# Kernel optimization log

Measured on AMD Instinct MI355X. Metric: run time of the kernel, lower is better.

Reference implementation:

```python
import jax, jax.numpy as jnp
import numpy as np
from jax import lax

HID = 512
NEG = -1e30

def conv2d(x, w, pad):
    # x: [N,C,H,W], w: [O,I,kh,kw]
    return lax.conv_general_dilated(x, w, (1, 1), [(pad, pad), (pad, pad)],
                                    dimension_numbers=('NCHW', 'OIHW', 'NCHW'))

def maxpool3s2p1(x):
    return lax.reduce_window(x, -jnp.inf, lax.max, (1, 1, 3, 3), (1, 1, 2, 2),
                             [(0, 0), (0, 0), (1, 1), (1, 1)])

def setup_inputs() -> dict:
    key = jax.random.key(0)
    ks = jax.random.split(key, 12)
    N, B = 128, 16
    gid = jnp.repeat(jnp.arange(B), N // B).astype(jnp.float32)  # sorted group ids
    rois = jnp.concatenate([gid[:, None], jax.random.uniform(ks[0], (N, 4))], axis=1)
    interact_feat = jax.random.normal(ks[1], (N, 2304, 1, 16, 16), jnp.float32)
    bbox_feat = jax.random.normal(ks[2], (N, 1024, 4, 7, 7), jnp.float32)
    s = lambda k, sh: jax.random.normal(k, sh, jnp.float32) * 0.02
    return {
        'rois': rois,
        'interact_feat': interact_feat,
        'bbox_feat': bbox_feat,
        'w_reduce': s(ks[3], (HID, 2304, 1, 1)),
        'w_rsize': s(ks[4], (HID, HID, 3, 3)),
        'wq': s(ks[5], (HID, HID, 3, 3)),
        'wk': s(ks[6], (HID, HID, 3, 3)),
        'wv': s(ks[7], (HID, HID, 3, 3)),
        'w1': s(ks[8], (HID, HID, 3, 3)),
        'gamma': jnp.ones((HID,), jnp.float32),
        'beta': jnp.zeros((HID,), jnp.float32),
        'w_fc': s(ks[9], (HID, 2 * HID)),
    }

def reference(rois, interact_feat, bbox_feat, w_reduce, w_rsize, wq, wk, wv, w1, gamma, beta, w_fc):
    f = interact_feat[:, :, 0]                      # squeeze(2): [N,2304,16,16]
    f = jax.nn.relu(conv2d(f, w_reduce, 0))         # [N,512,16,16]
    f = conv2d(f, w_rsize, 0)                       # no padding -> [N,512,14,14]
    f = maxpool3s2p1(f)                             # [N,512,7,7]

    gid = rois[:, 0].astype(jnp.int32)
    mask = gid[:, None] == gid[None, :]             # [N,N] same-group mask (vectorizes ragged loop)

    q = conv2d(f, wq, 1)
    k = conv2d(f, wk, 1)
    v = conv2d(f, wv, 1)
    # per-pixel attention across rois within each group
    att = jnp.einsum('ichw,jchw->ijhw', q, k) / jnp.sqrt(jnp.asarray(HID, f.dtype))
    att = jnp.where(mask[:, :, None, None], att, NEG)
    att = jax.nn.softmax(att, axis=1)               # softmax over key rois (dim=1)
    virt = jnp.einsum('ijhw,jchw->ichw', att, v)    # [N,512,7,7]

    # GroupNorm(1, C): normalize over (C,H,W), per-channel affine
    mu = virt.mean(axis=(1, 2, 3), keepdims=True)
    var = virt.var(axis=(1, 2, 3), keepdims=True)
    virt = (virt - mu) / jnp.sqrt(var + 1e-5)
    virt = virt * gamma[None, :, None, None] + beta[None, :, None, None]
    virt = jax.nn.relu(virt)
    virt = conv2d(virt, w1, 1)                      # dropout = identity in eval

    ho = (f + virt).mean(axis=(2, 3))               # gap1 -> [N,512]
    ob = bbox_feat.mean(axis=(2, 3, 4))             # gap2 -> [N,1024]
    ob = jax.nn.relu(ob @ w_fc.T)                   # fc1 -> [N,512]
    return jnp.concatenate([ho, ob], axis=1)        # [N,1024]
```

## Files before the change

### kernel.cpp

```cpp
#include <hip/hip_runtime.h>
#include <hip/hip_bf16.h>
#include <math.h>

typedef __bf16 bf16;
typedef __bf16 v8bf __attribute__((ext_vector_type(8)));
typedef float f32x4 __attribute__((ext_vector_type(4)));

#define GLDS16(g, l) __builtin_amdgcn_global_load_lds( \
    (const __attribute__((address_space(1))) void*)(g), \
    (__attribute__((address_space(3))) void*)(l), 16, 0, 0)

__device__ __forceinline__ int xcd_swz(int bid, int nwg) {
  int xcd = bid & 7, off = bid >> 3;
  int q = nwg >> 3, r = nwg & 7;
  return (xcd < r ? xcd * (q + 1) : r * (q + 1) + (xcd - r) * q) + off;
}

#define RING_COMPUTE() do { \
  v8bf b_[4], a_[4]; \
  _Pragma("unroll") for (int _j = 0; _j < 4; ++_j) { \
    int _lr = _j * 16 + l15; \
    int _c = (wn * 64 + colb) ^ ((_lr & 7) << 4); \
    b_[_j] = *(const v8bf*)(s0 + 16384 + _lr * 128 + _c); } \
  _Pragma("unroll") for (int _i = 0; _i < 4; ++_i) { \
    int _lr = _i * 16 + l15; \
    int _c = (wm * 64 + colb) ^ ((_lr & 7) << 4); \
    a_[_i] = *(const v8bf*)(s0 + _lr * 128 + _c); } \
  __builtin_amdgcn_s_setprio(1); \
  _Pragma("unroll") for (int _i = 0; _i < 4; ++_i) \
  _Pragma("unroll") for (int _j = 0; _j < 4; ++_j) \
    acc[_i][_j] = __builtin_amdgcn_mfma_f32_16x16x32_bf16(a_[_i], b_[_j], acc[_i][_j], 0, 0, 0); \
  __builtin_amdgcn_s_setprio(0); \
  _Pragma("unroll") for (int _i = 0; _i < 4; ++_i) { \
    int _lr = (_i + 4) * 16 + l15; \
    int _c = (wm * 64 + colb) ^ ((_lr & 7) << 4); \
    a_[_i] = *(const v8bf*)(s0 + _lr * 128 + _c); } \
  __builtin_amdgcn_s_setprio(1); \
  _Pragma("unroll") for (int _i = 0; _i < 4; ++_i) \
  _Pragma("unroll") for (int _j = 0; _j < 4; ++_j) \
    acc[_i + 4][_j] = __builtin_amdgcn_mfma_f32_16x16x32_bf16(a_[_i], b_[_j], acc[_i + 4][_j], 0, 0, 0); \
  __builtin_amdgcn_s_setprio(0); \
} while (0)

#define RING_LOOP(NG, STAGE) do { \
  STAGE(0, s0); STAGE(1, s1); \
  for (int g = 0; g < (NG); ++g) { \
    if (g + 2 < (NG)) { STAGE(g + 2, s2); } \
    if (g + 2 < (NG))       asm volatile("s_waitcnt vmcnt(12)" ::: "memory"); \
    else if (g + 2 == (NG)) asm volatile("s_waitcnt vmcnt(6)" ::: "memory"); \
    else                    asm volatile("s_waitcnt vmcnt(0)" ::: "memory"); \
    __builtin_amdgcn_s_barrier(); \
    __builtin_amdgcn_sched_barrier(0); \
    RING_COMPUTE(); \
    __builtin_amdgcn_sched_barrier(0); \
    __builtin_amdgcn_s_barrier(); \
    char* _tmp = s0; s0 = s1; s1 = s2; s2 = _tmp; \
  } \
} while (0)

__global__ __launch_bounds__(256, 2)
void k_gemm_reduce(const bf16* __restrict__ A, const bf16* __restrict__ B,
                   bf16* __restrict__ f1, int mbase)
{
  __shared__ __attribute__((aligned(16))) char lds[73728];
  char *s0 = lds, *s1 = lds + 24576, *s2 = lds + 49152;
  const int s = xcd_swz(blockIdx.x, gridDim.x);
  const int by = s & 3, bx = s >> 2;
  const int t = threadIdx.x, lane = t & 63, w = t >> 6;
  const int wm = w >> 1, wn = w & 1;
  const int l15 = lane & 15, colb = (lane >> 4) << 4;
  const int tr = t >> 3;
  const int lb = ((t & 7) << 4) ^ ((tr & 7) << 4);
  const int hi = lb >> 6, kb = lb & 63;
  const int t16 = t * 16;
  const char* pa[4]; const char* pb[2];
  #pragma unroll
  for (int i = 0; i < 4; ++i)
    pa[i] = (const char*)A + (size_t)(bx * 256 + i * 32 + tr + hi * 128) * 4608 + kb;
  #pragma unroll
  for (int i = 0; i < 2; ++i)
    pb[i] = (const char*)B + (size_t)(by * 128 + i * 32 + tr + hi * 64) * 4608 + kb;
  #define SG(kt, ring) do { \
    _Pragma("unroll") for (int _i = 0; _i < 4; ++_i) \
      GLDS16(pa[_i] + (size_t)(kt) * 64, (ring) + _i * 4096 + t16); \
    _Pragma("unroll") for (int _i = 0; _i < 2; ++_i) \
      GLDS16(pb[_i] + (size_t)(kt) * 64, (ring) + 16384 + _i * 4096 + t16); } while (0)
  f32x4 acc[8][4] = {};
  RING_LOOP(72, SG);
  const int rbase = (lane >> 4) << 2, cl = lane & 15;
  #pragma unroll
  for (int i = 0; i < 8; ++i)
    #pragma unroll
    for (int j = 0; j < 4; ++j)
      #pragma unroll
      for (int r = 0; r < 4; ++r) {
        int row = mbase + bx * 256 + wm * 128 + i * 16 + rbase + r;
        int col = by * 128 + wn * 64 + j * 16 + cl;
        f1[(size_t)row * 512 + col] = (bf16)fmaxf(acc[i][j][r], 0.f);
      }
}

__global__ __launch_bounds__(256, 2)
void k_conv_rsize(const bf16* __restrict__ f1, const bf16* __restrict__ wt,
                  bf16* __restrict__ f14)
{
  __shared__ __attribute__((aligned(16))) char lds[73728];
  char *s0 = lds, *s1 = lds + 24576, *s2 = lds + 49152;
  const int s = xcd_swz(blockIdx.x, gridDim.x);
  const int by = s & 3, bx = s >> 2;
  const int t = threadIdx.x, lane = t & 63, w = t >> 6;
  const int wm = w >> 1, wn = w & 1;
  const int l15 = lane & 15, colb = (lane >> 4) << 4;
  const int tr = t >> 3;
  const int lb = ((t & 7) << 4) ^ ((tr & 7) << 4);
  const int hi = lb >> 6, kb = lb & 63;
  const int t16 = t * 16;
  int abase[4]; const char* pb[2];
  #pragma unroll
  for (int i = 0; i < 4; ++i) {
    int m = bx * 256 + i * 32 + tr + hi * 128;
    int n = m / 196, rem = m - n * 196;
    int y = rem / 14, x = rem - 14 * (rem / 14);
    abase[i] = n * 256 + y * 16 + x;
  }
  #pragma unroll
  for (int i = 0; i < 2; ++i)
    pb[i] = (const char*)wt + (size_t)(by * 128 + i * 32 + tr + hi * 64) * 1024 + kb;
  const char* f1c = (const char*)f1 + kb;
  #define SC(kt, ring) do { int _tap = (kt) >> 4, _ko = ((kt) & 15) << 6; \
    int _dy = (_tap * 11) >> 5, _dx = _tap - _dy * 3; \
    int _df = (_dy * 16 + _dx) << 10; \
    _Pragma("unroll") for (int _i = 0; _i < 4; ++_i) \
      GLDS16(f1c + ((size_t)abase[_i] << 10) + _df + _ko, (ring) + _i * 4096 + t16); \
    _Pragma("unroll") for (int _i = 0; _i < 2; ++_i) \
      GLDS16(pb[_i] + (size_t)_tap * 524288 + _ko, (ring) + 16384 + _i * 4096 + t16); } while (0)
  f32x4 acc[8][4] = {};
  RING_LOOP(144, SC);
  const int rbase = (lane >> 4) << 2, cl = lane & 15;
  #pragma unroll
  for (int i = 0; i < 8; ++i)
    #pragma unroll
    for (int j = 0; j < 4; ++j)
      #pragma unroll
      for (int r = 0; r < 4; ++r) {
        int row = bx * 256 + wm * 128 + i * 16 + rbase + r;
        int col = by * 128 + wn * 64 + j * 16 + cl;
        f14[(size_t)row * 512 + col] = (bf16)acc[i][j][r];
      }
}

__global__ __launch_bounds__(256, 2)
void k_conv_qkv(const bf16* __restrict__ fin, const bf16* __restrict__ wt,
                bf16* __restrict__ qkv, const bf16* __restrict__ zp,
                const float* __restrict__ bbox, float* __restrict__ obm)
{
  __shared__ __attribute__((aligned(16))) char lds[73728];
  char *s0 = lds, *s1 = lds + 24576, *s2 = lds + 49152;
  const int t = threadIdx.x;
  if (blockIdx.x >= 300) {
    int bid = blockIdx.x - 300;
    int n = bid >> 4;
    int c = (bid & 15) * 64 + (t >> 2);
    int seg = t & 3;
    const float4* p4 = (const float4*)(bbox + ((size_t)n * 1024 + c) * 196);
    float sum = 0.f;
    for (int k = seg; k < 49; k += 4) { float4 ww = p4[k]; sum += ww.x + ww.y + ww.z + ww.w; }
    sum += __shfl_xor(sum, 1);
    sum += __shfl_xor(sum, 2);
    if (seg == 0) obm[n * 1024 + c] = sum * (1.f / 196.f);
    return;
  }
  const int s = xcd_swz(blockIdx.x, 300);
  const int q12 = s % 12, bx = s / 12;
  const int tensor = q12 >> 2, byl = q12 & 3;
  const char* wtc = (const char*)wt + (size_t)tensor * 4718592;
  bf16* outp = qkv + (size_t)tensor * 3211264;
  const int lane = t & 63, w = t >> 6;
  const int wm = w >> 1, wn = w & 1;
  const int l15 = lane & 15, colb = (lane >> 4) << 4;
  const int tr = t >> 3;
  const int lb = ((t & 7) << 4) ^ ((tr & 7) << 4);
  const int hi = lb >> 6, kb = lb & 63;
  const int t16 = t * 16;
  int nb[4], py[4], px[4]; const char* pb[2];
  #pragma unroll
  for (int i = 0; i < 4; ++i) {
    int m = bx * 256 + i * 32 + tr + hi * 128;
    if (m > 6271) m = 6271;
    int n = m / 49, rem = m - n * 49;
    nb[i] = n * 49;
    py[i] = rem / 7 - 1;
    px[i] = rem - 7 * (rem / 7) - 1;
  }
  #pragma unroll
  for (int i = 0; i < 2; ++i)
    pb[i] = wtc + (size_t)(byl * 128 + i * 32 + tr + hi * 64) * 1024 + kb;
  const char* finc = (const char*)fin + kb;
  const char* zpc = (const char*)zp;
  #define SQ(kt, ring) do { int _tap = (kt) >> 4, _ko = ((kt) & 15) << 6; \
    int _dy = (_tap * 11) >> 5, _dx = _tap - _dy * 3; \
    _Pragma("unroll") for (int _i = 0; _i < 4; ++_i) { \
      int _iy = py[_i] + _dy, _ix = px[_i] + _dx; \
      const char* _sp = ((unsigned)_iy < 7u && (unsigned)_ix < 7u) \
          ? finc + (size_t)(nb[_i] + _iy * 7 + _ix) * 1024 + _ko : zpc; \
      GLDS16(_sp, (ring) + _i * 4096 + t16); } \
    _Pragma("unroll") for (int _i = 0; _i < 2; ++_i) \
      GLDS16(pb[_i] + (size_t)_tap * 524288 + _ko, (ring) + 16384 + _i * 4096 + t16); } while (0)
  f32x4 acc[8][4] = {};
  RING_LOOP(144, SQ);
  const int rbase = (lane >> 4) << 2, cl = lane & 15;
  #pragma unroll
  for (int i = 0; i < 8; ++i)
    #pragma unroll
    for (int j = 0; j < 4; ++j)
      #pragma unroll
      for (int r = 0; r < 4; ++r) {
        int row = bx * 256 + wm * 128 + i * 16 + rbase + r;
        if (row < 6272) {
          int col = byl * 128 + wn * 64 + j * 16 + cl;
          outp[(size_t)row * 512 + col] = (bf16)acc[i][j][r];
        }
      }
}

__device__ __forceinline__ void tile_compute(const char* ldsA, const char* ldsB,
                                             f32x4 (&acc)[4][4], int wr, int wc, int lane) {
  const int l15 = lane & 15;
  const int colb = (lane >> 4) << 4;
  #pragma unroll
  for (int kk = 0; kk < 2; ++kk) {
    v8bf a[4], b[4];
    #pragma unroll
    for (int i = 0; i < 4; ++i) {
      int ra = wr * 64 + i * 16 + l15;
      int ca = ((kk << 6) | colb) ^ ((ra & 7) << 4);
      a[i] = *(const v8bf*)(ldsA + ra * 128 + ca);
    }
    #pragma unroll
    for (int j = 0; j < 4; ++j) {
      int rb = wc * 64 + j * 16 + l15;
      int cb = ((kk << 6) | colb) ^ ((rb & 7) << 4);
      b[j] = *(const v8bf*)(ldsB + rb * 128 + cb);
    }
    __builtin_amdgcn_s_setprio(1);
    #pragma unroll
    for (int i = 0; i < 4; ++i)
      #pragma unroll
      for (int j = 0; j < 4; ++j)
        acc[i][j] = __builtin_amdgcn_mfma_f32_16x16x32_bf16(a[i], b[j], acc[i][j], 0, 0, 0);
    __builtin_amdgcn_s_setprio(0);
  }
}

#define PIPELINE_LOOP(NK)                                                   \
  stage(0, lds);                                                            \
  stage(1, lds + 32768);                                                    \
  int cur = 0;                                                              \
  for (int ks = 0; ks < (NK) - 1; ++ks) {                                   \
    asm volatile("s_waitcnt vmcnt(8)" ::: "memory");                        \
    __builtin_amdgcn_s_barrier();                                           \
    __builtin_amdgcn_sched_barrier(0);                                      \
    tile_compute(lds + cur * 32768, lds + cur * 32768 + 16384, acc, wr, wc, lane); \
    __builtin_amdgcn_sched_barrier(0);                                      \
    __builtin_amdgcn_s_barrier();                                           \
    __builtin_amdgcn_sched_barrier(0);                                      \
    if (ks + 2 < (NK)) stage(ks + 2, lds + cur * 32768);                    \
    cur ^= 1;                                                               \
  }                                                                         \
  asm volatile("s_waitcnt vmcnt(0)" ::: "memory");                          \
  __builtin_amdgcn_s_barrier();                                             \
  __builtin_amdgcn_sched_barrier(0);                                        \
  tile_compute(lds + cur * 32768, lds + cur * 32768 + 16384, acc, wr, wc, lane);

__global__ __launch_bounds__(256)
void k_gemm_s(const bf16* __restrict__ A_s, const bf16* __restrict__ w1r,
              float* __restrict__ part)
{
  __shared__ __attribute__((aligned(16))) char lds[65536];
  const int by = blockIdx.x, kspl = blockIdx.y;
  const int t = threadIdx.x, lane = t & 63, w = t >> 6, wr = w >> 1, wc = w & 1;
  const int tr = t >> 3;
  const int cphys = ((t & 7) << 4) ^ ((tr & 7) << 4);
  const char* pa[4]; const char* pb[4];
  #pragma unroll
  for (int i = 0; i < 4; ++i) {
    int r = i * 32 + tr;
    pa[i] = (const char*)A_s + (size_t)r * 9216 + kspl * 2304 + cphys;
    pb[i] = (const char*)w1r + (size_t)(by * 128 + r) * 9216 + kspl * 2304 + cphys;
  }
  const int lo = t * 16;
  auto stage = [&](int ks, char* base) {
    #pragma unroll
    for (int i = 0; i < 4; ++i) GLDS16(pa[i] + ks * 128, base + lo + i * 4096);
    #pragma unroll
    for (int i = 0; i < 4; ++i) GLDS16(pb[i] + ks * 128, base + 16384 + lo + i * 4096);
  };
  f32x4 acc[4][4] = {};
  PIPELINE_LOOP(18)
  const int rb = (lane >> 4) << 2, cl = lane & 15;
  #pragma unroll
  for (int i = 0; i < 4; ++i)
    #pragma unroll
    for (int j = 0; j < 4; ++j)
      #pragma unroll
      for (int r = 0; r < 4; ++r) {
        int row = wr * 64 + i * 16 + rb + r;
        int col = by * 128 + wc * 64 + j * 16 + cl;
        part[(size_t)kspl * 65536 + row * 512 + col] = acc[i][j][r];
      }
}

__global__ __launch_bounds__(512)
void k_red(const float* __restrict__ part, const float* __restrict__ f7m,
           float* __restrict__ out)
{
  int idx = blockIdx.x * 512 + threadIdx.x;
  float s = part[idx] + part[65536 + idx] + part[131072 + idx] + part[196608 + idx];
  int row = idx >> 9, col = idx & 511;
  out[row * 1024 + col] = s + f7m[idx];
}

__global__ void k_tin(const float* __restrict__ in, bf16* __restrict__ A1, int n0)
{
  __shared__ float tile[64][36];
  const int k0 = blockIdx.x * 64, p0 = blockIdx.y * 32, nl = blockIdx.z;
  const int n = n0 + nl;
  const int t = threadIdx.x;
  const float* src = in + (size_t)n * 2304 * 256;
  #pragma unroll
  for (int rep = 0; rep < 2; ++rep) {
    int idx = t + rep * 256;
    int row = idx >> 3, c4 = (idx & 7) * 4;
    float4 v = *(const float4*)(src + (size_t)(k0 + row) * 256 + p0 + c4);
    tile[row][c4] = v.x; tile[row][c4 + 1] = v.y;
    tile[row][c4 + 2] = v.z; tile[row][c4 + 3] = v.w;
  }
  __syncthreads();
  const int pl = t >> 3, ke = (t & 7) * 8;
  v8bf o;
  #pragma unroll
  for (int e = 0; e < 8; ++e) o[e] = (bf16)tile[ke + e][pl];
  bf16* dst = A1 + (size_t)nl * 256 * 2304;
  *(v8bf*)(dst + (size_t)(p0 + pl) * 2304 + k0 + ke) = o;
}

__global__ void k_wprep(const float* __restrict__ wred, const float* __restrict__ s0,
                        const float* __restrict__ s1, const float* __restrict__ s2,
                        const float* __restrict__ s3, const float* __restrict__ s4,
                        bf16* __restrict__ wrb, bf16* __restrict__ wt,
                        bf16* __restrict__ w1r)
{
  if (blockIdx.x < 1152) {
    int idx = (blockIdx.x * 256 + threadIdx.x) * 4;
    float4 v = *(const float4*)(wred + idx);
    bf16* d = wrb + idx;
    d[0] = (bf16)v.x; d[1] = (bf16)v.y; d[2] = (bf16)v.z; d[3] = (bf16)v.w;
    return;
  }
  int bid = blockIdx.x - 1152;
  int by = bid >> 10, bx = bid & 1023;
  const float* src;
  switch (by) {
    case 0: src = s0; break; case 1: src = s1; break; case 2: src = s2; break;
    case 3: src = s3; break; default: src = s4; break;
  }
  int q = bx * 256 + threadIdx.x;
  const float* sp = src + (size_t)q * 9;
  float tmp[9];
  #pragma unroll
  for (int e = 0; e < 9; ++e) tmp[e] = sp[e];
  if (by < 4) {
    bf16* dst = wt + (size_t)by * 2359296;
    #pragma unroll
    for (int e = 0; e < 9; ++e) dst[(size_t)e * 262144 + q] = (bf16)tmp[e];
  } else {
    int co = q >> 9, ci = q & 511;
    #pragma unroll
    for (int e = 0; e < 9; ++e) w1r[(size_t)(co * 9 + e) * 512 + ci] = (bf16)tmp[e];
  }
}

__global__ void k_pool(const bf16* __restrict__ f14, bf16* __restrict__ f7b)
{
  int idx = blockIdx.x * 256 + threadIdx.x;
  int c2 = idx & 255;
  int pp = idx >> 8;
  int n = pp / 49, p7 = pp - n * 49;
  int y = p7 / 7, x = p7 - 7 * (p7 / 7);
  int y0 = 2 * y - 1, x0 = 2 * x - 1;
  const unsigned* f14u = (const unsigned*)f14;
  float m0 = -3.4e38f, m1 = -3.4e38f;
  #pragma unroll
  for (int dy = 0; dy < 3; ++dy) {
    int iy = y0 + dy; if ((unsigned)iy >= 14u) continue;
    #pragma unroll
    for (int dx = 0; dx < 3; ++dx) {
      int ix = x0 + dx; if ((unsigned)ix >= 14u) continue;
      unsigned vv = f14u[(size_t)(n * 196 + iy * 14 + ix) * 256 + c2];
      m0 = fmaxf(m0, __builtin_bit_cast(float, vv << 16));
      m1 = fmaxf(m1, __builtin_bit_cast(float, vv & 0xffff0000u));
    }
  }
  bf16 b0 = (bf16)m0, b1 = (bf16)m1;
  unsigned pk = (unsigned)__builtin_bit_cast(unsigned short, b0)
              | ((unsigned)__builtin_bit_cast(unsigned short, b1) << 16);
  ((unsigned*)f7b)[idx] = pk;
}

__global__ __launch_bounds__(256)
void k_attn(const bf16* __restrict__ q, const bf16* __restrict__ k,
            const bf16* __restrict__ v, const float* __restrict__ rois,
            float* __restrict__ virt)
{
  const int p = blockIdx.x, g = blockIdx.y, t = threadIdx.x;
  __shared__ float sS[8][9];
  __shared__ float sP[8][9];
  __shared__ __attribute__((aligned(16))) bf16 sV[8][512];
  {
    int u = t;
    #pragma unroll
    for (int rep = 0; rep < 2; ++rep, u += 256) {
      int j = u >> 6, ch = u & 63;
      *(v8bf*)&sV[j][ch * 8] = *(const v8bf*)(v + ((size_t)(g * 8 + j) * 49 + p) * 512 + ch * 8);
    }
  }
  int pi = t >> 2, ls = t & 3;
  int i = pi >> 3, j = pi & 7;
  const bf16* qi = q + ((size_t)(g * 8 + i) * 49 + p) * 512;
  const bf16* kj = k + ((size_t)(g * 8 + j) * 49 + p) * 512;
  float s = 0.f;
  for (int ch = ls * 16; ch < ls * 16 + 16; ++ch) {
    v8bf a = *(const v8bf*)(qi + ch * 8);
    v8bf b = *(const v8bf*)(kj + ch * 8);
    #pragma unroll
    for (int e = 0; e < 8; ++e) s += (float)a[e] * (float)b[e];
  }
  s += __shfl_xor(s, 1);
  s += __shfl_xor(s, 2);
  if (ls == 0) sS[i][j] = s * 0.04419417382415922f;
  __syncthreads();
  if (t < 8) {
    float gi = rois[(g * 8 + t) * 5];
    float pv[8]; float mx = -3.4e38f;
    #pragma unroll
    for (int jj = 0; jj < 8; ++jj) {
      float gj = rois[(g * 8 + jj) * 5];
      float sv = (gi == gj) ? sS[t][jj] : -1e30f;
      pv[jj] = sv; mx = fmaxf(mx, sv);
    }
    float sum = 0.f;
    #pragma unroll
    for (int jj = 0; jj < 8; ++jj) { float e = expf(pv[jj] - mx); pv[jj] = e; sum += e; }
    float inv = 1.f / sum;
    #pragma unroll
    for (int jj = 0; jj < 8; ++jj) sP[t][jj] = pv[jj] * inv;
  }
  __syncthreads();
  int i2 = t >> 5, c0 = (t & 31) * 16;
  float o[16];
  #pragma unroll
  for (int e = 0; e < 16; ++e) o[e] = 0.f;
  #pragma unroll
  for (int jj = 0; jj < 8; ++jj) {
    float ww = sP[i2][jj];
    v8bf v0 = *(const v8bf*)&sV[jj][c0];
    v8bf v1 = *(const v8bf*)&sV[jj][c0 + 8];
    #pragma unroll
    for (int e = 0; e < 8; ++e) { o[e] += ww * (float)v0[e]; o[8 + e] += ww * (float)v1[e]; }
  }
  float* dst = virt + ((size_t)(g * 8 + i2) * 49 + p) * 512 + c0;
  #pragma unroll
  for (int e = 0; e < 16; ++e) dst[e] = o[e];
}

__global__ __launch_bounds__(512)
void k_ln_fc(const float* __restrict__ virt, const float* __restrict__ gamma,
             const float* __restrict__ beta, const bf16* __restrict__ f7b,
             bf16* __restrict__ A_s, float* __restrict__ f7m,
             const float* __restrict__ obm, const float* __restrict__ wfc,
             float* __restrict__ out)
{
  const int t = threadIdx.x;
  if (blockIdx.x >= 128) {
    __shared__ float sO[1024];
    int n = blockIdx.x - 128;
    for (int u = t; u < 1024; u += 512) sO[u] = obm[n * 1024 + u];
    __syncthreads();
    const float4* wp = (const float4*)(wfc + (size_t)t * 1024);
    float s = 0.f;
    for (int c4 = 0; c4 < 256; ++c4) {
      float4 w = wp[c4];
      s += w.x * sO[c4 * 4] + w.y * sO[c4 * 4 + 1] + w.z * sO[c4 * 4 + 2] + w.w * sO[c4 * 4 + 3];
    }
    out[n * 1024 + 512 + t] = fmaxf(s, 0.f);
    return;
  }
  const int n = blockIdx.x;
  const float* p = virt + (size_t)n * 25088 + t;
  float xv[49];
  float s1 = 0.f, s2 = 0.f;
  #pragma unroll
  for (int pp = 0; pp < 49; ++pp) {
    float x = p[pp * 512];
    xv[pp] = x; s1 += x; s2 += x * x;
  }
  __shared__ float r1[512], r2[512];
  r1[t] = s1; r2[t] = s2; __syncthreads();
  for (int off = 256; off; off >>= 1) {
    if (t < off) { r1[t] += r1[t + off]; r2[t] += r2[t + off]; }
    __syncthreads();
  }
  float mu = r1[0] * (1.f / 25088.f);
  float var = r2[0] * (1.f / 25088.f) - mu * mu;
  float rstd = rsqrtf(var + 1e-5f);
  float g = gamma[t], be = beta[t];
  const bf16* fp = f7b + (size_t)n * 25088 + t;
  float T = 0, R0 = 0, R6 = 0, C0 = 0, C6 = 0;
  float X00 = 0, X06 = 0, X60 = 0, X66 = 0, F = 0;
  #pragma unroll
  for (int pp = 0; pp < 49; ++pp) {
    const int u = pp / 7, v = pp - 7 * (pp / 7);
    float y = fmaxf((xv[pp] - mu) * rstd * g + be, 0.f);
    T += y;
    if (u == 0) R0 += y;
    if (u == 6) R6 += y;
    if (v == 0) C0 += y;
    if (v == 6) C6 += y;
    if (pp == 0)  X00 = y;
    if (pp == 6)  X06 = y;
    if (pp == 42) X60 = y;
    if (pp == 48) X66 = y;
    F += (float)fp[pp * 512];
  }
  float sv[9] = { T-R6-C6+X66, T-R6, T-R6-C0+X60,
                  T-C6,        T,    T-C0,
                  T-R0-C6+X06, T-R0, T-R0-C0+X00 };
  bf16* Ap = A_s + (size_t)n * 4608 + t;
  #pragma unroll
  for (int tap = 0; tap < 9; ++tap)
    Ap[tap * 512] = (bf16)(sv[tap] * (1.f / 49.f));
  f7m[n * 512 + t] = F * (1.f / 49.f);
}

extern "C" void kernel_launch(void* const* d_in, const int* in_sizes, int n_in,
                              void* d_out, int out_size, void* d_ws, size_t ws_size,
                              hipStream_t stream) {
  const float* rois     = (const float*)d_in[0];
  const float* interact = (const float*)d_in[1];
  const float* bbox     = (const float*)d_in[2];
  const float* w_reduce = (const float*)d_in[3];
  const float* w_rsize  = (const float*)d_in[4];
  const float* wq       = (const float*)d_in[5];
  const float* wk       = (const float*)d_in[6];
  const float* wv       = (const float*)d_in[7];
  const float* w1       = (const float*)d_in[8];
  const float* gamma    = (const float*)d_in[9];
  const float* beta     = (const float*)d_in[10];
  const float* wfc      = (const float*)d_in[11];
  float* out = (float*)d_out;
  char* ws = (char*)d_ws;

  size_t o = 0;
  auto take = [&](size_t sz) { size_t r = o; o += (sz + 255) & ~(size_t)255; return r; };
  bf16*  wrb   = (bf16*)(ws + take(2359296));
  bf16*  wt    = (bf16*)(ws + take(18874368));
  bf16*  w1r   = (bf16*)(ws + take(4718592));
  char*  Rf1   = ws + take(33554432);
  bf16*  f7b   = (bf16*)(ws + take(6422528));
  float* virt  = (float*)(ws + take(12845056));
  bf16*  A_s   = (bf16*)(ws + take(1179648));
  float* f7m   = (float*)(ws + take(262144));
  float* part  = (float*)(ws + take(1048576));
  float* obm   = (float*)(ws + take(524288));
  bf16*  zp    = (bf16*)(ws + take(256));
  size_t fixedEnd = o;
  const size_t A1_FULL = 150994944;
  bool full = (ws_size >= fixedEnd + A1_FULL);
  bf16* A1  = (bf16*)(ws + fixedEnd);
  bf16* f14 = (bf16*)(ws + fixedEnd);

  bf16* f1 = (bf16*)Rf1;
  bf16* qb = (bf16*)Rf1;
  bf16* kb = qb + 3211264;
  bf16* vb = kb + 3211264;

  hipMemsetAsync(zp, 0, 256, stream);

  k_wprep<<<6272, 256, 0, stream>>>(w_reduce, w_rsize, wq, wk, wv, w1, wrb, wt, w1r);

  if (full) {
    k_tin<<<dim3(36, 8, 128), 256, 0, stream>>>(interact, A1, 0);
    k_gemm_reduce<<<512, 256, 0, stream>>>(A1, wrb, f1, 0);
  } else {
    for (int ch = 0; ch < 4; ++ch) {
      k_tin<<<dim3(36, 8, 32), 256, 0, stream>>>(interact, A1, ch * 32);
      k_gemm_reduce<<<128, 256, 0, stream>>>(A1, wrb, f1, ch * 8192);
    }
  }

  k_conv_rsize<<<392, 256, 0, stream>>>(f1, wt, f14);
  k_pool<<<6272, 256, 0, stream>>>(f14, f7b);

  k_conv_qkv<<<2348, 256, 0, stream>>>(f7b, wt + (size_t)1 * 2359296, qb, zp, bbox, obm);

  k_attn<<<dim3(49, 16), 256, 0, stream>>>(qb, kb, vb, rois, virt);

  k_ln_fc<<<256, 512, 0, stream>>>(virt, gamma, beta, f7b, A_s, f7m, obm, wfc, out);

  k_gemm_s<<<dim3(4, 4), 256, 0, stream>>>(A_s, w1r, part);
  k_red<<<128, 512, 0, stream>>>(part, f7m, out);
}
```

Measured before the change: 542.0 us.

## Rewrite reduce and rsize GEMMs with 256x256 tiles, 8 waves, phased double-buffer

```diff
diff --git a/kernel.cpp b/kernel.cpp
--- a/kernel.cpp
+++ b/kernel.cpp
@@ -14,6 +14,171 @@
   int xcd = bid & 7, off = bid >> 3;
   int q = nwg >> 3, r = nwg & 7;
   return (xcd < r ? xcd * (q + 1) : r * (q + 1) + (xcd - r) * q) + off;
+}
+
+#define SBZ __builtin_amdgcn_sched_barrier(0)
+#define BARR __builtin_amdgcn_s_barrier()
+
+#define RD_B8(SLOTB) do { \
+  _Pragma("unroll") for (int _j = 0; _j < 4; ++_j) \
+  _Pragma("unroll") for (int _kk = 0; _kk < 2; ++_kk) { \
+    int _r = (wn & 1) * 64 + _j * 16 + l15; \
+    int _c = (_kk * 64 + kq) ^ ((_r & 7) << 4); \
+    bfr[_j][_kk] = *(const v8bf*)((SLOTB) + _r * 128 + _c); } } while (0)
+
+#define RD_A4(SLOTA, CL) do { \
+  _Pragma("unroll") for (int _f = 0; _f < 2; ++_f) \
+  _Pragma("unroll") for (int _kk = 0; _kk < 2; ++_kk) { \
+    int _r = (CL) * 32 + _f * 16 + l15; \
+    int _c = (_kk * 64 + kq) ^ ((_r & 7) << 4); \
+    af[_f][_kk] = *(const v8bf*)((SLOTA) + _r * 128 + _c); } } while (0)
+
+#define MMA16(CL) do { \
+  __builtin_amdgcn_s_setprio(1); \
+  _Pragma("unroll") for (int _f = 0; _f < 2; ++_f) \
+  _Pragma("unroll") for (int _j = 0; _j < 4; ++_j) \
+  _Pragma("unroll") for (int _kk = 0; _kk < 2; ++_kk) \
+    acc[(CL)*2 + _f][_j] = __builtin_amdgcn_mfma_f32_16x16x32_bf16( \
+        af[_f][_kk], bfr[_j][_kk], acc[(CL)*2 + _f][_j], 0, 0, 0); \
+  __builtin_amdgcn_s_setprio(0); } while (0)
+
+#define VM4 asm volatile("s_waitcnt vmcnt(4)" ::: "memory")
+#define VM0 asm volatile("s_waitcnt vmcnt(0)" ::: "memory")
+
+#define PH8_ITER(STGA, STGB, NIT)                                        \
+  {                                                                      \
+    int t1k = 2 * iv + 1, t2k = 2 * iv + 2, t3k = 2 * iv + 3;            \
+    bool s2 = (iv + 1 < (NIT));                                          \
+    RD_B8(bslot0); RD_A4(aslot0, 0); STGA(0, t1k, 1);                    \
+    SBZ; BARR; SBZ; MMA16(0); SBZ; BARR;                                 \
+    RD_A4(aslot0, 1); STGA(1, t1k, 1);                                   \
+    SBZ; BARR; SBZ; MMA16(1); SBZ; BARR;                                 \
+    RD_A4(aslot0, 2); if (s2) STGB(0, t2k, 0);                           \
+    SBZ; BARR; SBZ; MMA16(2); SBZ; BARR;                                 \
+    RD_A4(aslot0, 3); if (s2) STGB(1, t2k, 0);                           \
+    SBZ; BARR; SBZ; MMA16(3); SBZ;                                       \
+    if (s2) { VM4; } else { VM0; }                                       \
+    BARR;                                                                \
+    RD_B8(bslot1); RD_A4(aslot1, 0); if (s2) STGA(0, t2k, 0);            \
+    SBZ; BARR; SBZ; MMA16(0); SBZ; BARR;                                 \
+    RD_A4(aslot1, 1); if (s2) STGA(1, t2k, 0);                           \
+    SBZ; BARR; SBZ; MMA16(1); SBZ; BARR;                                 \
+    RD_A4(aslot1, 2); if (s2) STGB(0, t3k, 1);                           \
+    SBZ; BARR; SBZ; MMA16(2); SBZ; BARR;                                 \
+    RD_A4(aslot1, 3); if (s2) STGB(1, t3k, 1);                           \
+    SBZ; BARR; SBZ; MMA16(3); SBZ;                                       \
+    if (s2) { VM4; } else { VM0; }                                       \
+    BARR;                                                                \
+  }
+
+__global__ __launch_bounds__(512, 2)
+void k_gemm_reduce(const bf16* __restrict__ A, const bf16* __restrict__ B,
+                   bf16* __restrict__ f1, int mbase)
+{
+  extern __shared__ char lds[];
+  const int s = xcd_swz(blockIdx.x, gridDim.x);
+  const int by = s & 1, bx = s >> 1;
+  const int t = threadIdx.x, lane = t & 63, w = t >> 6;
+  const int wm = w >> 2, wn = w & 3;
+  const int l15 = lane & 15, kq = (lane >> 4) << 4;
+  const int tr64 = t >> 3;
+  const int lb = ((t & 7) << 4) ^ ((tr64 & 7) << 4);
+  const int t16 = t * 16;
+  const char* aslot0 = lds + wm * 16384;
+  const char* aslot1 = lds + 65536 + wm * 16384;
+  const char* bslot0 = lds + 32768 + (wn >> 1) * 16384;
+  const char* bslot1 = lds + 98304 + (wn >> 1) * 16384;
+  const char* paA[2][2]; const char* paB[2][2];
+  #pragma unroll
+  for (int h = 0; h < 2; ++h)
+    #pragma unroll
+    for (int c = 0; c < 2; ++c) {
+      paA[h][c] = (const char*)A + (size_t)(bx * 256 + h * 128 + c * 64 + tr64) * 4608 + lb;
+      paB[h][c] = (const char*)B + (size_t)(by * 256 + h * 128 + c * 64 + tr64) * 4608 + lb;
+    }
+  #define GR_STGA(h, kt, d) do { \
+    GLDS16(paA[h][0] + (size_t)(kt) * 128, lds + (d) * 65536 + (h) * 16384 + t16); \
+    GLDS16(paA[h][1] + (size_t)(kt) * 128, lds + (d) * 65536 + (h) * 16384 + 8192 + t16); } while (0)
+  #define GR_STGB(h, kt, d) do { \
+    GLDS16(paB[h][0] + (size_t)(kt) * 128, lds + (d) * 65536 + 32768 + (h) * 16384 + t16); \
+    GLDS16(paB[h][1] + (size_t)(kt) * 128, lds + (d) * 65536 + 32768 + (h) * 16384 + 8192 + t16); } while (0)
+
+  f32x4 acc[8][4] = {};
+  v8bf bfr[4][2], af[2][2];
+  GR_STGB(0, 0, 0); GR_STGB(1, 0, 0); GR_STGA(0, 0, 0); GR_STGA(1, 0, 0);
+  GR_STGB(0, 1, 1); GR_STGB(1, 1, 1);
+  VM4; BARR;
+  for (int iv = 0; iv < 18; ++iv) PH8_ITER(GR_STGA, GR_STGB, 18);
+  const int rbase = (lane >> 4) << 2, cl = lane & 15;
+  #pragma unroll
+  for (int i = 0; i < 8; ++i)
+    #pragma unroll
+    for (int j = 0; j < 4; ++j)
+      #pragma unroll
+      for (int r = 0; r < 4; ++r) {
+        int row = mbase + bx * 256 + wm * 128 + i * 16 + rbase + r;
+        int col = by * 256 + wn * 64 + j * 16 + cl;
+        f1[(size_t)row * 512 + col] = (bf16)fmaxf(acc[i][j][r], 0.f);
+      }
+}
+
+__global__ __launch_bounds__(512, 2)
+void k_conv_rsize(const bf16* __restrict__ f1, const bf16* __restrict__ wt,
+                  bf16* __restrict__ f14)
+{
+  extern __shared__ char lds[];
+  const int s = xcd_swz(blockIdx.x, gridDim.x);
+  const int by = s & 1, bx = s >> 1;
+  const int t = threadIdx.x, lane = t & 63, w = t >> 6;
+  const int wm = w >> 2, wn = w & 3;
+  const int l15 = lane & 15, kq = (lane >> 4) << 4;
+  const int tr64 = t >> 3;
+  const int lb = ((t & 7) << 4) ^ ((tr64 & 7) << 4);
+  const int t16 = t * 16;
+  const char* aslot0 = lds + wm * 16384;
+  const char* aslot1 = lds + 65536 + wm * 16384;
+  const char* bslot0 = lds + 32768 + (wn >> 1) * 16384;
+  const char* bslot1 = lds + 98304 + (wn >> 1) * 16384;
+  int ab[2][2]; const char* pwB[2][2];
+  #pragma unroll
+  for (int h = 0; h < 2; ++h)
+    #pragma unroll
+    for (int c = 0; c < 2; ++c) {
+      int m = bx * 256 + h * 128 + c * 64 + tr64;
+      int n = m / 196, rem = m - n * 196;
+      int y = rem / 14, x = rem - 14 * (rem / 14);
+      ab[h][c] = n * 256 + y * 16 + x;
+      pwB[h][c] = (const char*)wt + (size_t)(by * 256 + h * 128 + c * 64 + tr64) * 1024 + lb;
+    }
+  const char* f1c = (const char*)f1 + lb;
+  #define CR_STGA(h, kt, d) do { \
+    int _tap = (kt) >> 3, _ko = ((kt) & 7) << 7; \
+    int _dy = (_tap * 11) >> 5, _dx = _tap - _dy * 3; \
+    int _df = (_dy * 16 + _dx) << 10; \
+    GLDS16(f1c + ((size_t)ab[h][0] << 10) + _df + _ko, lds + (d) * 65536 + (h) * 16384 + t16); \
+    GLDS16(f1c + ((size_t)ab[h][1] << 10) + _df + _ko, lds + (d) * 65536 + (h) * 16384 + 8192 + t16); } while (0)
+  #define CR_STGB(h, kt, d) do { \
+    int _tap = (kt) >> 3, _ko = ((kt) & 7) << 7; \
+    GLDS16(pwB[h][0] + (size_t)_tap * 524288 + _ko, lds + (d) * 65536 + 32768 + (h) * 16384 + t16); \
+    GLDS16(pwB[h][1] + (size_t)_tap * 524288 + _ko, lds + (d) * 65536 + 32768 + (h) * 16384 + 8192 + t16); } while (0)
+
+  f32x4 acc[8][4] = {};
+  v8bf bfr[4][2], af[2][2];
+  CR_STGB(0, 0, 0); CR_STGB(1, 0, 0); CR_STGA(0, 0, 0); CR_STGA(1, 0, 0);
+  CR_STGB(0, 1, 1); CR_STGB(1, 1, 1);
+  VM4; BARR;
+  for (int iv = 0; iv < 36; ++iv) PH8_ITER(CR_STGA, CR_STGB, 36);
+  const int rbase = (lane >> 4) << 2, cl = lane & 15;
+  #pragma unroll
+  for (int i = 0; i < 8; ++i)
+    #pragma unroll
+    for (int j = 0; j < 4; ++j)
+      #pragma unroll
+      for (int r = 0; r < 4; ++r) {
+        int row = bx * 256 + wm * 128 + i * 16 + rbase + r;
+        int col = by * 256 + wn * 64 + j * 16 + cl;
+        f14[(size_t)row * 512 + col] = (bf16)acc[i][j][r];
+      }
 }
 
 #define RING_COMPUTE() do { \
@@ -59,103 +224,12 @@
 } while (0)
 
 __global__ __launch_bounds__(256, 2)
-void k_gemm_reduce(const bf16* __restrict__ A, const bf16* __restrict__ B,
-                   bf16* __restrict__ f1, int mbase)
-{
-  __shared__ __attribute__((aligned(16))) char lds[73728];
-  char *s0 = lds, *s1 = lds + 24576, *s2 = lds + 49152;
-  const int s = xcd_swz(blockIdx.x, gridDim.x);
-  const int by = s & 3, bx = s >> 2;
-  const int t = threadIdx.x, lane = t & 63, w = t >> 6;
-  const int wm = w >> 1, wn = w & 1;
-  const int l15 = lane & 15, colb = (lane >> 4) << 4;
-  const int tr = t >> 3;
-  const int lb = ((t & 7) << 4) ^ ((tr & 7) << 4);
-  const int hi = lb >> 6, kb = lb & 63;
-  const int t16 = t * 16;
-  const char* pa[4]; const char* pb[2];
-  #pragma unroll
-  for (int i = 0; i < 4; ++i)
-    pa[i] = (const char*)A + (size_t)(bx * 256 + i * 32 + tr + hi * 128) * 4608 + kb;
-  #pragma unroll
-  for (int i = 0; i < 2; ++i)
-    pb[i] = (const char*)B + (size_t)(by * 128 + i * 32 + tr + hi * 64) * 4608 + kb;
-  #define SG(kt, ring) do { \
-    _Pragma("unroll") for (int _i = 0; _i < 4; ++_i) \
-      GLDS16(pa[_i] + (size_t)(kt) * 64, (ring) + _i * 4096 + t16); \
-    _Pragma("unroll") for (int _i = 0; _i < 2; ++_i) \
-      GLDS16(pb[_i] + (size_t)(kt) * 64, (ring) + 16384 + _i * 4096 + t16); } while (0)
-  f32x4 acc[8][4] = {};
-  RING_LOOP(72, SG);
-  const int rbase = (lane >> 4) << 2, cl = lane & 15;
-  #pragma unroll
-  for (int i = 0; i < 8; ++i)
-    #pragma unroll
-    for (int j = 0; j < 4; ++j)
-      #pragma unroll
-      for (int r = 0; r < 4; ++r) {
-        int row = mbase + bx * 256 + wm * 128 + i * 16 + rbase + r;
-        int col = by * 128 + wn * 64 + j * 16 + cl;
-        f1[(size_t)row * 512 + col] = (bf16)fmaxf(acc[i][j][r], 0.f);
-      }
-}
-
-__global__ __launch_bounds__(256, 2)
-void k_conv_rsize(const bf16* __restrict__ f1, const bf16* __restrict__ wt,
-                  bf16* __restrict__ f14)
-{
-  __shared__ __attribute__((aligned(16))) char lds[73728];
-  char *s0 = lds, *s1 = lds + 24576, *s2 = lds + 49152;
-  const int s = xcd_swz(blockIdx.x, gridDim.x);
-  const int by = s & 3, bx = s >> 2;
-  const int t = threadIdx.x, lane = t & 63, w = t >> 6;
-  const int wm = w >> 1, wn = w & 1;
-  const int l15 = lane & 15, colb = (lane >> 4) << 4;
-  const int tr = t >> 3;
-  const int lb = ((t & 7) << 4) ^ ((tr & 7) << 4);
-  const int hi = lb >> 6, kb = lb & 63;
-  const int t16 = t * 16;
-  int abase[4]; const char* pb[2];
-  #pragma unroll
-  for (int i = 0; i < 4; ++i) {
-    int m = bx * 256 + i * 32 + tr + hi * 128;
-    int n = m / 196, rem = m - n * 196;
-    int y = rem / 14, x = rem - 14 * (rem / 14);
-    abase[i] = n * 256 + y * 16 + x;
-  }
-  #pragma unroll
-  for (int i = 0; i < 2; ++i)
-    pb[i] = (const char*)wt + (size_t)(by * 128 + i * 32 + tr + hi * 64) * 1024 + kb;
-  const char* f1c = (const char*)f1 + kb;
-  #define SC(kt, ring) do { int _tap = (kt) >> 4, _ko = ((kt) & 15) << 6; \
-    int _dy = (_tap * 11) >> 5, _dx = _tap - _dy * 3; \
-    int _df = (_dy * 16 + _dx) << 10; \
-    _Pragma("unroll") for (int _i = 0; _i < 4; ++_i) \
-      GLDS16(f1c + ((size_t)abase[_i] << 10) + _df + _ko, (ring) + _i * 4096 + t16); \
-    _Pragma("unroll") for (int _i = 0; _i < 2; ++_i) \
-      GLDS16(pb[_i] + (size_t)_tap * 524288 + _ko, (ring) + 16384 + _i * 4096 + t16); } while (0)
-  f32x4 acc[8][4] = {};
-  RING_LOOP(144, SC);
-  const int rbase = (lane >> 4) << 2, cl = lane & 15;
-  #pragma unroll
-  for (int i = 0; i < 8; ++i)
-    #pragma unroll
-    for (int j = 0; j < 4; ++j)
-      #pragma unroll
-      for (int r = 0; r < 4; ++r) {
-        int row = bx * 256 + wm * 128 + i * 16 + rbase + r;
-        int col = by * 128 + wn * 64 + j * 16 + cl;
-        f14[(size_t)row * 512 + col] = (bf16)acc[i][j][r];
-      }
-}
-
-__global__ __launch_bounds__(256, 2)
 void k_conv_qkv(const bf16* __restrict__ fin, const bf16* __restrict__ wt,
                 bf16* __restrict__ qkv, const bf16* __restrict__ zp,
                 const float* __restrict__ bbox, float* __restrict__ obm)
 {
-  __shared__ __attribute__((aligned(16))) char lds[73728];
-  char *s0 = lds, *s1 = lds + 24576, *s2 = lds + 49152;
+  __shared__ __attribute__((aligned(16))) char ldss[73728];
+  char *s0 = ldss, *s1 = ldss + 24576, *s2 = ldss + 49152;
   const int t = threadIdx.x;
   if (blockIdx.x >= 300) {
     int bid = blockIdx.x - 300;
@@ -590,15 +664,15 @@
 
   if (full) {
     k_tin<<<dim3(36, 8, 128), 256, 0, stream>>>(interact, A1, 0);
-    k_gemm_reduce<<<512, 256, 0, stream>>>(A1, wrb, f1, 0);
+    k_gemm_reduce<<<256, 512, 131072, stream>>>(A1, wrb, f1, 0);
   } else {
     for (int ch = 0; ch < 4; ++ch) {
       k_tin<<<dim3(36, 8, 32), 256, 0, stream>>>(interact, A1, ch * 32);
-      k_gemm_reduce<<<128, 256, 0, stream>>>(A1, wrb, f1, ch * 8192);
-    }
-  }
-
-  k_conv_rsize<<<392, 256, 0, stream>>>(f1, wt, f14);
+      k_gemm_reduce<<<64, 512, 131072, stream>>>(A1, wrb, f1, ch * 8192);
+    }
+  }
+
+  k_conv_rsize<<<196, 512, 131072, stream>>>(f1, wt, f14);
   k_pool<<<6272, 256, 0, stream>>>(f14, f7b);
 
   k_conv_qkv<<<2348, 256, 0, stream>>>(f7b, wt + (size_t)1 * 2359296, qb, zp, bbox, obm);
```

Result: faster. 516.3 us (-4.7%).
